# Kernel tuning notes

Measured on AMD Instinct MI355X. Metric: run time of the kernel, lower is better.

## Reference

```python
import jax, jax.numpy as jnp
import numpy as np

TEMPERATURE = 0.1  # init arg `temperature`


def _l2_normalize(x):
    return x / jnp.sqrt(jnp.sum(x * x, axis=1, keepdims=True))


def setup_inputs() -> dict:
    key = jax.random.key(0)
    k1, k2, k3 = jax.random.split(key, 3)
    B, D, Q = 2048, 128, 65536
    projections_1 = jax.random.normal(k1, (B, D), dtype=jnp.float32)
    projections_2 = jax.random.normal(k2, (B, D), dtype=jnp.float32)
    # queue is initialized row-l2-normalized in the original module
    feature_queue = _l2_normalize(jax.random.normal(k3, (Q, D), dtype=jnp.float32))
    return {"projections_1": projections_1, "projections_2": projections_2,
            "feature_queue": feature_queue}


def reference(projections_1, projections_2, feature_queue):
    # NNCLR.contrastive_loss (per-sample losses), including nearest_neighbour.
    p1 = _l2_normalize(projections_1)  # [B, D]
    p2 = _l2_normalize(projections_2)  # [B, D]

    def nearest_neighbour(p):
        # [B, Q] similarity -> top-1 index -> gather from queue
        sims = jnp.einsum('bd,qd->bq', p, feature_queue)
        idx = jnp.argmax(sims, axis=1)  # [B]
        nn = feature_queue[idx]         # [B, D]
        # straight-through: value = nn, gradient flows to p
        return p + jax.lax.stop_gradient(nn - p)

    nn1 = nearest_neighbour(p1)
    nn2 = nearest_neighbour(p2)

    s_1_2_1 = jnp.einsum('id,jd->ij', nn1, p2) / TEMPERATURE
    s_1_2_2 = jnp.einsum('id,jd->ij', p2, nn1) / TEMPERATURE
    s_2_1_1 = jnp.einsum('id,jd->ij', nn2, p1) / TEMPERATURE
    s_2_1_2 = jnp.einsum('id,jd->ij', p1, nn2) / TEMPERATURE

    logits = jnp.concatenate([s_1_2_1, s_1_2_2, s_2_1_1, s_2_1_2], axis=0)  # [4B, B]
    B = p1.shape[0]
    labels = jnp.tile(jnp.arange(B), 4)  # [4B]
    logp = jax.nn.log_softmax(logits, axis=1)
    loss = -jnp.take_along_axis(logp, labels[:, None], axis=1)[:, 0]  # [4B]
    return loss
```

## Files before the change

kernel.cpp:

```cpp
#include <hip/hip_runtime.h>

#define S 132
#define SCALE 10.0f
#define EPS_MARGIN 0.008f
#define SROWS_CAP 480
#define ROWCHUNK 48
#define RC_MAX 10
#define STRIP_CAND 256

typedef __attribute__((ext_vector_type(8))) short short8;
typedef __attribute__((ext_vector_type(4))) float floatx4;

#define MFMA16(a, b, c) __builtin_amdgcn_mfma_f32_16x16x32_bf16((a), (b), (c), 0, 0, 0)

__device__ __forceinline__ unsigned int ordered_bits(float f) {
    unsigned int b = __float_as_uint(f);
    return (b & 0x80000000u) ? ~b : (b | 0x80000000u);
}
__device__ __forceinline__ float from_ordered(unsigned int u) {
    return __uint_as_float((u & 0x80000000u) ? (u ^ 0x80000000u) : ~u);
}
__device__ __forceinline__ short bf_rne(float x) {
    unsigned int u = __float_as_uint(x);
    return (short)((u + 0x7FFFu + ((u >> 16) & 1u)) >> 16);
}
__device__ __forceinline__ float bf2f(short s) {
    return __uint_as_float(((unsigned int)(unsigned short)s) << 16);
}

__global__ void k_prep(const float* __restrict__ p1, const float* __restrict__ p2,
                       float* __restrict__ pn, short* __restrict__ pnb,
                       unsigned int* __restrict__ mbest,
                       unsigned long long* __restrict__ best,
                       unsigned int* __restrict__ scnt,
                       float* __restrict__ sums) {
    int row = blockIdx.x;
    int t = threadIdx.x;
    const float* src = (row < 2048) ? (p1 + (size_t)row * 128)
                                    : (p2 + (size_t)(row - 2048) * 128);
    float2 v = ((const float2*)src)[t];
    float ss = v.x * v.x + v.y * v.y;
    #pragma unroll
    for (int o = 32; o; o >>= 1) ss += __shfl_xor(ss, o);
    float inv = 1.0f / sqrtf(ss);
    float2 o2; o2.x = v.x * inv; o2.y = v.y * inv;
    ((float2*)(pn + (size_t)row * 128))[t] = o2;
    unsigned int pk = (unsigned int)(unsigned short)bf_rne(o2.x)
                    | ((unsigned int)(unsigned short)bf_rne(o2.y) << 16);
    ((unsigned int*)(pnb + (size_t)row * 128))[t] = pk;
    if (t == 0) { mbest[row] = 0u; best[row] = 0ULL; if (row < 1024) scnt[row] = 0u; }
    if (row < 128) sums[row * 64 + t] = 0.0f;
}

__global__ void k_qcvt(const float* __restrict__ queue, short* __restrict__ qb) {
    size_t i = ((size_t)blockIdx.x * 256 + threadIdx.x) * 8;
    float4 f0 = *(const float4*)(queue + i);
    float4 f1 = *(const float4*)(queue + i + 4);
    short8 o;
    o[0] = bf_rne(f0.x); o[1] = bf_rne(f0.y); o[2] = bf_rne(f0.z); o[3] = bf_rne(f0.w);
    o[4] = bf_rne(f1.x); o[5] = bf_rne(f1.y); o[6] = bf_rne(f1.z); o[7] = bf_rne(f1.w);
    *(short8*)(qb + i) = o;
}

__device__ __forceinline__ void screen_tile(const short8 A[8][4],
                                            short8 b0, short8 b1, short8 b2, short8 b3,
                                            float rmax[8][4]) {
    floatx4 acc[8];
    floatx4 zero = {0.0f, 0.0f, 0.0f, 0.0f};
    #pragma unroll
    for (int rf = 0; rf < 8; ++rf) acc[rf] = MFMA16(A[rf][0], b0, zero);
    #pragma unroll
    for (int rf = 0; rf < 8; ++rf) acc[rf] = MFMA16(A[rf][1], b1, acc[rf]);
    #pragma unroll
    for (int rf = 0; rf < 8; ++rf) acc[rf] = MFMA16(A[rf][2], b2, acc[rf]);
    #pragma unroll
    for (int rf = 0; rf < 8; ++rf) acc[rf] = MFMA16(A[rf][3], b3, acc[rf]);
    #pragma unroll
    for (int rf = 0; rf < 8; ++rf)
        #pragma unroll
        for (int r = 0; r < 4; ++r) rmax[rf][r] = fmaxf(rmax[rf][r], acc[rf][r]);
}

__global__ __launch_bounds__(256, 2) void k_screen(const short* __restrict__ pnb,
                                                   const short* __restrict__ qb,
                                                   unsigned int* __restrict__ mbest,
                                                   float* __restrict__ smax) {
    int tid = threadIdx.x;
    int lane = tid & 63, wv = tid >> 6;
    int n16 = lane & 15, quad = lane >> 4;

    int id = blockIdx.x;
    int xcd = id & 7;
    int g = id >> 3;
    int rowblk = g & 7;
    int qsub = g >> 3;
    int qsplit = xcd * 8 + qsub;
    int rowbase = rowblk * 512 + wv * 128;
    int qstart = qsplit * 1024;

    short8 A[8][4];
    #pragma unroll
    for (int rf = 0; rf < 8; ++rf) {
        const short* ap = pnb + (size_t)(rowbase + rf * 16 + n16) * 128 + quad * 8;
        #pragma unroll
        for (int kk = 0; kk < 4; ++kk)
            A[rf][kk] = *(const short8*)(ap + kk * 32);
    }

    float rmax[8][4];
    #pragma unroll
    for (int rf = 0; rf < 8; ++rf)
        #pragma unroll
        for (int r = 0; r < 4; ++r) rmax[rf][r] = -1e30f;

    const short* lp = qb + (size_t)(qstart + n16) * 128 + quad * 8;
    short8 a0 = *(const short8*)(lp), a1 = *(const short8*)(lp + 32),
           a2 = *(const short8*)(lp + 64), a3 = *(const short8*)(lp + 96);

    for (int t = 0; t < 64; t += 2) {
        if ((t & 15) == 0) __syncthreads();
        const short* p1p = lp + 2048;
        short8 b0 = *(const short8*)(p1p), b1 = *(const short8*)(p1p + 32),
               b2 = *(const short8*)(p1p + 64), b3 = *(const short8*)(p1p + 96);
        screen_tile(A, a0, a1, a2, a3, rmax);
        const short* p2p = lp + 4096;
        a0 = *(const short8*)(p2p); a1 = *(const short8*)(p2p + 32);
        a2 = *(const short8*)(p2p + 64); a3 = *(const short8*)(p2p + 96);
        screen_tile(A, b0, b1, b2, b3, rmax);
        lp += 4096;
    }

    #pragma unroll
    for (int rf = 0; rf < 8; ++rf)
        #pragma unroll
        for (int r = 0; r < 4; ++r) {
            float v = rmax[rf][r];
            v = fmaxf(v, __shfl_xor(v, 1));
            v = fmaxf(v, __shfl_xor(v, 2));
            v = fmaxf(v, __shfl_xor(v, 4));
            v = fmaxf(v, __shfl_xor(v, 8));
            if (n16 == 0) {
                int row = rowbase + rf * 16 + quad * 4 + r;
                atomicMax(&mbest[row], ordered_bits(v));
                smax[(size_t)qsplit * 4096 + row] = v;
            }
        }
}

__global__ __launch_bounds__(256) void k_rows(const unsigned int* __restrict__ mbest,
                                              const float* __restrict__ smax,
                                              int* __restrict__ rcnt,
                                              unsigned short* __restrict__ rlist) {
    __shared__ unsigned short rows[SROWS_CAP];
    __shared__ int nsh;
    int tid = threadIdx.x;
    int s = blockIdx.x;
    if (tid == 0) nsh = 0;
    __syncthreads();
    const float* sm = smax + (size_t)s * 4096;
    #pragma unroll
    for (int j = 0; j < 16; ++j) {
        int row = tid + 256 * j;
        float thr = from_ordered(mbest[row]) - EPS_MARGIN;
        if (sm[row] > thr) {
            int pos = atomicAdd(&nsh, 1);
            if (pos < SROWS_CAP) rows[pos] = (unsigned short)row;
        }
    }
    __syncthreads();
    int n = nsh; if (n > SROWS_CAP) n = SROWS_CAP;
    if (tid == 0) rcnt[s] = n;
    for (int i = tid; i < n; i += 256) rlist[s * SROWS_CAP + i] = rows[i];
}

__global__ __launch_bounds__(256, 4) void k_rescreen(const short* __restrict__ pnb,
                                                     const short* __restrict__ qb,
                                                     const unsigned int* __restrict__ mbest,
                                                     const int* __restrict__ rcnt,
                                                     const unsigned short* __restrict__ rlist,
                                                     unsigned int* __restrict__ scnt,
                                                     unsigned int* __restrict__ cand) {
    int b = blockIdx.x;
    int s = b & 63;
    int qp = (b >> 6) & 15;
    int rc = b >> 10;
    int n = rcnt[s];
    int base = rc * ROWCHUNK;
    if (base >= n) return;

    int tid = threadIdx.x;
    int lane = tid & 63, wv = tid >> 6;
    int n16 = lane & 15, quad = lane >> 4;
    int qt = qp * 4 + wv;
    int qrow = s * 1024 + qt * 16 + n16;

    const short* bp = qb + (size_t)qrow * 128 + quad * 8;
    short8 b0 = *(const short8*)(bp);
    short8 b1 = *(const short8*)(bp + 32);
    short8 b2 = *(const short8*)(bp + 64);
    short8 b3 = *(const short8*)(bp + 96);

    const unsigned short* rl = rlist + s * SROWS_CAP;
    short8 Af[3][4]; float th[3][4]; int rowC[3][4];
    #pragma unroll
    for (int rt = 0; rt < 3; ++rt) {
        int ia = base + rt * 16 + n16;
        int rA = rl[ia < n ? ia : base];
        const short* ap = pnb + (size_t)rA * 128 + quad * 8;
        #pragma unroll
        for (int kk = 0; kk < 4; ++kk) Af[rt][kk] = *(const short8*)(ap + kk * 32);
        #pragma unroll
        for (int r = 0; r < 4; ++r) {
            int ic = base + rt * 16 + quad * 4 + r;
            if (ic < n) {
                int rr = rl[ic];
                rowC[rt][r] = rr;
                th[rt][r] = from_ordered(mbest[rr]) - EPS_MARGIN;
            } else { rowC[rt][r] = 0; th[rt][r] = 3.0e38f; }
        }
    }
    #pragma unroll
    for (int rt = 0; rt < 3; ++rt) {
        floatx4 zero = {0.0f, 0.0f, 0.0f, 0.0f};
        floatx4 acc = MFMA16(Af[rt][0], b0, zero);
        acc = MFMA16(Af[rt][1], b1, acc);
        acc = MFMA16(Af[rt][2], b2, acc);
        acc = MFMA16(Af[rt][3], b3, acc);
        #pragma unroll
        for (int r = 0; r < 4; ++r) {
            if (acc[r] > th[rt][r]) {
                unsigned int pos = atomicAdd(&scnt[s * 16], 1u);
                if (pos < STRIP_CAND)
                    cand[s * STRIP_CAND + pos] =
                        ((unsigned int)rowC[rt][r] << 16) | (unsigned int)(qrow & 0xFFFF);
            }
        }
    }
}

__global__ void k_rerank(const float* __restrict__ pn, const float* __restrict__ queue,
                         const unsigned int* __restrict__ scnt,
                         const unsigned int* __restrict__ cand,
                         unsigned long long* __restrict__ best) {
    int widx = (blockIdx.x * 256 + threadIdx.x) >> 6;
    int lane = threadIdx.x & 63;
    int s = widx >> 8, slot = widx & 255;
    unsigned int c = scnt[s * 16]; if (c > STRIP_CAND) c = STRIP_CAND;
    if ((unsigned int)slot >= c) return;
    unsigned int v = cand[s * STRIP_CAND + slot];
    unsigned int row = v >> 16;
    unsigned int q = (unsigned int)(s * 1024) + (v & 0x3FFu);
    q = (unsigned int)(s * 1024) + ((v & 0xFFFFu) - (unsigned int)(s * 1024 & 0xFFFF));
    q = v & 0xFFFFu;
    float2 a = ((const float2*)(pn + (size_t)row * 128))[lane];
    float2 b = ((const float2*)(queue + (size_t)q * 128))[lane];
    float d = a.x * b.x + a.y * b.y;
    #pragma unroll
    for (int o = 32; o; o >>= 1) d += __shfl_xor(d, o);
    if (lane == 0) {
        unsigned long long pk = ((unsigned long long)ordered_bits(d) << 32)
                              | (unsigned long long)(unsigned int)(~q);
        atomicMax(&best[row], pk);
    }
}

__global__ void k_gather(const float* __restrict__ queue,
                         const unsigned long long* __restrict__ best,
                         short* __restrict__ nnb) {
    int row = blockIdx.x;
    int t = threadIdx.x;
    unsigned int idx = ~(unsigned int)(best[row] & 0xFFFFFFFFull);
    idx &= 0xFFFFu;
    float2 v = ((const float2*)(queue + (size_t)idx * 128))[t];
    unsigned int pk = (unsigned int)(unsigned short)bf_rne(v.x)
                    | ((unsigned int)(unsigned short)bf_rne(v.y) << 16);
    ((unsigned int*)(nnb + (size_t)row * 128))[t] = pk;
}

__global__ __launch_bounds__(256) void k_gemm_lse(const short* __restrict__ Ab,
                                                  const float* __restrict__ B,
                                                  float* __restrict__ rowsum,
                                                  float* __restrict__ colsum,
                                                  float* __restrict__ diag) {
    __shared__ __align__(16) float al[64 * S];
    __shared__ __align__(16) float bl[64 * S];
    __shared__ float red[64][17];
    int tid = threadIdx.x;
    const short8* asrc = (const short8*)(Ab + (size_t)blockIdx.x * 64 * 128);
    #pragma unroll
    for (int i = tid; i < 1024; i += 256) {
        short8 v = asrc[i];
        int r = i >> 4, c = (i & 15) * 8;
        float* dst = &al[r * S + c];
        #pragma unroll
        for (int j = 0; j < 8; ++j) dst[j] = bf2f(v[j]);
    }
    const float4* bsrc = (const float4*)(B + (size_t)blockIdx.y * 64 * 128);
    #pragma unroll
    for (int i = tid; i < 2048; i += 256) {
        int r = i >> 5, c = i & 31;
        *(float4*)&bl[r * S + c * 4] = bsrc[i];
    }
    __syncthreads();
    int ty = tid >> 4, tx = tid & 15;
    float acc[4][4] = {};
    #pragma unroll 2
    for (int k = 0; k < 128; k += 4) {
        float4 a[4], b[4];
        #pragma unroll
        for (int i = 0; i < 4; ++i) a[i] = *(const float4*)&al[(ty + 16 * i) * S + k];
        #pragma unroll
        for (int j = 0; j < 4; ++j) b[j] = *(const float4*)&bl[(tx + 16 * j) * S + k];
        #pragma unroll
        for (int i = 0; i < 4; ++i)
            #pragma unroll
            for (int j = 0; j < 4; ++j)
                acc[i][j] += a[i].x * b[j].x + a[i].y * b[j].y +
                             a[i].z * b[j].z + a[i].w * b[j].w;
    }
    int rowbase = blockIdx.x * 64, colbase = blockIdx.y * 64;

    float e[4][4], rs[4], cs[4];
    #pragma unroll
    for (int i = 0; i < 4; ++i) { rs[i] = 0.0f; cs[i] = 0.0f; }
    #pragma unroll
    for (int i = 0; i < 4; ++i)
        #pragma unroll
        for (int j = 0; j < 4; ++j) {
            e[i][j] = __expf(acc[i][j] * SCALE - 10.0f);
            rs[i] += e[i][j];
        }
    #pragma unroll
    for (int j = 0; j < 4; ++j)
        #pragma unroll
        for (int i = 0; i < 4; ++i) cs[j] += e[i][j];

    if (rowbase == colbase && ty == tx) {
        #pragma unroll
        for (int i = 0; i < 4; ++i) diag[rowbase + ty + 16 * i] = acc[i][i];
    }

    #pragma unroll
    for (int i = 0; i < 4; ++i) red[ty + 16 * i][tx] = rs[i];
    __syncthreads();
    if (tid < 64) {
        float s = 0.0f;
        #pragma unroll
        for (int x = 0; x < 16; ++x) s += red[tid][x];
        atomicAdd(&rowsum[rowbase + tid], s);
    }
    __syncthreads();
    #pragma unroll
    for (int j = 0; j < 4; ++j) red[tx + 16 * j][ty] = cs[j];
    __syncthreads();
    if (tid < 64) {
        float s = 0.0f;
        #pragma unroll
        for (int x = 0; x < 16; ++x) s += red[tid][x];
        atomicAdd(&colsum[colbase + tid], s);
    }
}

__global__ void k_final(const float* __restrict__ sums,
                        const float* __restrict__ dg1, const float* __restrict__ dg2,
                        float* __restrict__ out) {
    int idx = blockIdx.x * 256 + threadIdx.x;
    int seg = idx >> 11, r = idx & 2047;
    float s = sums[seg * 2048 + r];
    float d = (seg < 2) ? dg1[r] : dg2[r];
    out[idx] = 10.0f + logf(s) - d * SCALE;
}

extern "C" void kernel_launch(void* const* d_in, const int* in_sizes, int n_in,
                              void* d_out, int out_size, void* d_ws, size_t ws_size,
                              hipStream_t stream) {
    const float* p1    = (const float*)d_in[0];
    const float* p2    = (const float*)d_in[1];
    const float* queue = (const float*)d_in[2];
    float* out = (float*)d_out;

    char* w = (char*)d_ws;
    float* pn  = (float*)w;
    short* nnb = (short*)(w + (2u << 20));
    short* qb  = (short*)(w + (3u << 20));
    short* pnb = (short*)(w + (19u << 20));
    char* b2 = w + (20u << 20);
    unsigned int* mbest = (unsigned int*)b2;
    unsigned long long* best = (unsigned long long*)(b2 + (16u << 10));
    unsigned int* scnt = (unsigned int*)(b2 + (48u << 10));
    int* rcnt = (int*)(b2 + (52u << 10));
    unsigned short* rlist = (unsigned short*)(b2 + (56u << 10));
    unsigned int* cand = (unsigned int*)(b2 + (116u << 10));
    float* sums = (float*)(b2 + (180u << 10));
    float* dg1  = sums + 8192;
    float* dg2  = dg1 + 2048;
    float* smax = (float*)nnb;

    k_prep<<<4096, 64, 0, stream>>>(p1, p2, pn, pnb, mbest, best, scnt, sums);
    k_qcvt<<<4096, 256, 0, stream>>>(queue, qb);
    k_screen<<<512, 256, 0, stream>>>(pnb, qb, mbest, smax);
    k_rows<<<64, 256, 0, stream>>>(mbest, smax, rcnt, rlist);
    k_rescreen<<<64 * 16 * RC_MAX, 256, 0, stream>>>(pnb, qb, mbest, rcnt, rlist, scnt, cand);
    k_rerank<<<4096, 256, 0, stream>>>(pn, queue, scnt, cand, best);
    k_gather<<<4096, 64, 0, stream>>>(queue, best, nnb);

    k_gemm_lse<<<dim3(32, 32), 256, 0, stream>>>(nnb, pn + 2048 * 128,
                                                 sums, sums + 2048, dg1);
    k_gemm_lse<<<dim3(32, 32), 256, 0, stream>>>(nnb + 2048 * 128, pn,
                                                 sums + 4096, sums + 6144, dg2);
    k_final<<<32, 256, 0, stream>>>(sums, dg1, dg2, out);
}
```

Baseline: 247.2 us.

## Rebalance screen, rescreen and rerank grids for occupancy and fewer empty blocks

Result: slower. 302.8 us (+22.5%).

```diff
diff --git a/kernel.cpp b/kernel.cpp
--- a/kernel.cpp
+++ b/kernel.cpp
@@ -5,7 +5,6 @@
 #define EPS_MARGIN 0.008f
 #define SROWS_CAP 480
 #define ROWCHUNK 48
-#define RC_MAX 10
 #define STRIP_CAND 256
 
 typedef __attribute__((ext_vector_type(8))) short short8;
@@ -62,26 +61,7 @@
     *(short8*)(qb + i) = o;
 }
 
-__device__ __forceinline__ void screen_tile(const short8 A[8][4],
-                                            short8 b0, short8 b1, short8 b2, short8 b3,
-                                            float rmax[8][4]) {
-    floatx4 acc[8];
-    floatx4 zero = {0.0f, 0.0f, 0.0f, 0.0f};
-    #pragma unroll
-    for (int rf = 0; rf < 8; ++rf) acc[rf] = MFMA16(A[rf][0], b0, zero);
-    #pragma unroll
-    for (int rf = 0; rf < 8; ++rf) acc[rf] = MFMA16(A[rf][1], b1, acc[rf]);
-    #pragma unroll
-    for (int rf = 0; rf < 8; ++rf) acc[rf] = MFMA16(A[rf][2], b2, acc[rf]);
-    #pragma unroll
-    for (int rf = 0; rf < 8; ++rf) acc[rf] = MFMA16(A[rf][3], b3, acc[rf]);
-    #pragma unroll
-    for (int rf = 0; rf < 8; ++rf)
-        #pragma unroll
-        for (int r = 0; r < 4; ++r) rmax[rf][r] = fmaxf(rmax[rf][r], acc[rf][r]);
-}
-
-__global__ __launch_bounds__(256, 2) void k_screen(const short* __restrict__ pnb,
+__global__ __launch_bounds__(256, 4) void k_screen(const short* __restrict__ pnb,
                                                    const short* __restrict__ qb,
                                                    unsigned int* __restrict__ mbest,
                                                    float* __restrict__ smax) {
@@ -92,46 +72,57 @@
     int id = blockIdx.x;
     int xcd = id & 7;
     int g = id >> 3;
-    int rowblk = g & 7;
-    int qsub = g >> 3;
+    int qsub = g & 7;
+    int rowblk = g >> 3;
     int qsplit = xcd * 8 + qsub;
-    int rowbase = rowblk * 512 + wv * 128;
+    int rowbase = rowblk * 256 + wv * 64;
     int qstart = qsplit * 1024;
 
-    short8 A[8][4];
-    #pragma unroll
-    for (int rf = 0; rf < 8; ++rf) {
+    short8 A[4][4];
+    #pragma unroll
+    for (int rf = 0; rf < 4; ++rf) {
         const short* ap = pnb + (size_t)(rowbase + rf * 16 + n16) * 128 + quad * 8;
         #pragma unroll
         for (int kk = 0; kk < 4; ++kk)
             A[rf][kk] = *(const short8*)(ap + kk * 32);
     }
 
-    float rmax[8][4];
-    #pragma unroll
-    for (int rf = 0; rf < 8; ++rf)
+    float rmax[4][4];
+    #pragma unroll
+    for (int rf = 0; rf < 4; ++rf)
         #pragma unroll
         for (int r = 0; r < 4; ++r) rmax[rf][r] = -1e30f;
 
     const short* lp = qb + (size_t)(qstart + n16) * 128 + quad * 8;
-    short8 a0 = *(const short8*)(lp), a1 = *(const short8*)(lp + 32),
-           a2 = *(const short8*)(lp + 64), a3 = *(const short8*)(lp + 96);
-
-    for (int t = 0; t < 64; t += 2) {
-        if ((t & 15) == 0) __syncthreads();
-        const short* p1p = lp + 2048;
-        short8 b0 = *(const short8*)(p1p), b1 = *(const short8*)(p1p + 32),
-               b2 = *(const short8*)(p1p + 64), b3 = *(const short8*)(p1p + 96);
-        screen_tile(A, a0, a1, a2, a3, rmax);
-        const short* p2p = lp + 4096;
-        a0 = *(const short8*)(p2p); a1 = *(const short8*)(p2p + 32);
-        a2 = *(const short8*)(p2p + 64); a3 = *(const short8*)(p2p + 96);
-        screen_tile(A, b0, b1, b2, b3, rmax);
-        lp += 4096;
-    }
-
-    #pragma unroll
-    for (int rf = 0; rf < 8; ++rf)
+    for (int tb = 0; tb < 4; ++tb) {
+        __syncthreads();
+        #pragma unroll 1
+        for (int ti = 0; ti < 16; ++ti) {
+            short8 b0 = *(const short8*)(lp);
+            short8 b1 = *(const short8*)(lp + 32);
+            short8 b2 = *(const short8*)(lp + 64);
+            short8 b3 = *(const short8*)(lp + 96);
+            floatx4 acc[4];
+            floatx4 zero = {0.0f, 0.0f, 0.0f, 0.0f};
+            #pragma unroll
+            for (int rf = 0; rf < 4; ++rf) acc[rf] = MFMA16(A[rf][0], b0, zero);
+            #pragma unroll
+            for (int rf = 0; rf < 4; ++rf) acc[rf] = MFMA16(A[rf][1], b1, acc[rf]);
+            #pragma unroll
+            for (int rf = 0; rf < 4; ++rf) acc[rf] = MFMA16(A[rf][2], b2, acc[rf]);
+            #pragma unroll
+            for (int rf = 0; rf < 4; ++rf) acc[rf] = MFMA16(A[rf][3], b3, acc[rf]);
+            #pragma unroll
+            for (int rf = 0; rf < 4; ++rf)
+                #pragma unroll
+                for (int r = 0; r < 4; ++r)
+                    rmax[rf][r] = fmaxf(rmax[rf][r], acc[rf][r]);
+            lp += 2048;
+        }
+    }
+
+    #pragma unroll
+    for (int rf = 0; rf < 4; ++rf)
         #pragma unroll
         for (int r = 0; r < 4; ++r) {
             float v = rmax[rf][r];
@@ -182,11 +173,9 @@
                                                      unsigned int* __restrict__ cand) {
     int b = blockIdx.x;
     int s = b & 63;
-    int qp = (b >> 6) & 15;
-    int rc = b >> 10;
+    int qp = b >> 6;
     int n = rcnt[s];
-    int base = rc * ROWCHUNK;
-    if (base >= n) return;
+    if (n == 0) return;
 
     int tid = threadIdx.x;
     int lane = tid & 63, wv = tid >> 6;
@@ -201,38 +190,40 @@
     short8 b3 = *(const short8*)(bp + 96);
 
     const unsigned short* rl = rlist + s * SROWS_CAP;
-    short8 Af[3][4]; float th[3][4]; int rowC[3][4];
-    #pragma unroll
-    for (int rt = 0; rt < 3; ++rt) {
-        int ia = base + rt * 16 + n16;
-        int rA = rl[ia < n ? ia : base];
-        const short* ap = pnb + (size_t)rA * 128 + quad * 8;
-        #pragma unroll
-        for (int kk = 0; kk < 4; ++kk) Af[rt][kk] = *(const short8*)(ap + kk * 32);
-        #pragma unroll
-        for (int r = 0; r < 4; ++r) {
-            int ic = base + rt * 16 + quad * 4 + r;
-            if (ic < n) {
-                int rr = rl[ic];
-                rowC[rt][r] = rr;
-                th[rt][r] = from_ordered(mbest[rr]) - EPS_MARGIN;
-            } else { rowC[rt][r] = 0; th[rt][r] = 3.0e38f; }
-        }
-    }
-    #pragma unroll
-    for (int rt = 0; rt < 3; ++rt) {
-        floatx4 zero = {0.0f, 0.0f, 0.0f, 0.0f};
-        floatx4 acc = MFMA16(Af[rt][0], b0, zero);
-        acc = MFMA16(Af[rt][1], b1, acc);
-        acc = MFMA16(Af[rt][2], b2, acc);
-        acc = MFMA16(Af[rt][3], b3, acc);
-        #pragma unroll
-        for (int r = 0; r < 4; ++r) {
-            if (acc[r] > th[rt][r]) {
-                unsigned int pos = atomicAdd(&scnt[s * 16], 1u);
-                if (pos < STRIP_CAND)
-                    cand[s * STRIP_CAND + pos] =
-                        ((unsigned int)rowC[rt][r] << 16) | (unsigned int)(qrow & 0xFFFF);
+    for (int base = 0; base < n; base += ROWCHUNK) {
+        short8 Af[3][4]; float th[3][4]; int rowC[3][4];
+        #pragma unroll
+        for (int rt = 0; rt < 3; ++rt) {
+            int ia = base + rt * 16 + n16;
+            int rA = rl[ia < n ? ia : base];
+            const short* ap = pnb + (size_t)rA * 128 + quad * 8;
+            #pragma unroll
+            for (int kk = 0; kk < 4; ++kk) Af[rt][kk] = *(const short8*)(ap + kk * 32);
+            #pragma unroll
+            for (int r = 0; r < 4; ++r) {
+                int ic = base + rt * 16 + quad * 4 + r;
+                if (ic < n) {
+                    int rr = rl[ic];
+                    rowC[rt][r] = rr;
+                    th[rt][r] = from_ordered(mbest[rr]) - EPS_MARGIN;
+                } else { rowC[rt][r] = 0; th[rt][r] = 3.0e38f; }
+            }
+        }
+        #pragma unroll
+        for (int rt = 0; rt < 3; ++rt) {
+            floatx4 zero = {0.0f, 0.0f, 0.0f, 0.0f};
+            floatx4 acc = MFMA16(Af[rt][0], b0, zero);
+            acc = MFMA16(Af[rt][1], b1, acc);
+            acc = MFMA16(Af[rt][2], b2, acc);
+            acc = MFMA16(Af[rt][3], b3, acc);
+            #pragma unroll
+            for (int r = 0; r < 4; ++r) {
+                if (acc[r] > th[rt][r]) {
+                    unsigned int pos = atomicAdd(&scnt[s * 16], 1u);
+                    if (pos < STRIP_CAND)
+                        cand[s * STRIP_CAND + pos] =
+                            ((unsigned int)rowC[rt][r] << 16) | (unsigned int)(qrow & 0xFFFF);
+                }
             }
         }
     }
@@ -242,25 +233,24 @@
                          const unsigned int* __restrict__ scnt,
                          const unsigned int* __restrict__ cand,
                          unsigned long long* __restrict__ best) {
-    int widx = (blockIdx.x * 256 + threadIdx.x) >> 6;
-    int lane = threadIdx.x & 63;
-    int s = widx >> 8, slot = widx & 255;
+    int lane = threadIdx.x & 63, wv = threadIdx.x >> 6;
+    int s = blockIdx.x >> 2;
+    int wq = ((blockIdx.x & 3) << 2) | wv;
     unsigned int c = scnt[s * 16]; if (c > STRIP_CAND) c = STRIP_CAND;
-    if ((unsigned int)slot >= c) return;
-    unsigned int v = cand[s * STRIP_CAND + slot];
-    unsigned int row = v >> 16;
-    unsigned int q = (unsigned int)(s * 1024) + (v & 0x3FFu);
-    q = (unsigned int)(s * 1024) + ((v & 0xFFFFu) - (unsigned int)(s * 1024 & 0xFFFF));
-    q = v & 0xFFFFu;
-    float2 a = ((const float2*)(pn + (size_t)row * 128))[lane];
-    float2 b = ((const float2*)(queue + (size_t)q * 128))[lane];
-    float d = a.x * b.x + a.y * b.y;
-    #pragma unroll
-    for (int o = 32; o; o >>= 1) d += __shfl_xor(d, o);
-    if (lane == 0) {
-        unsigned long long pk = ((unsigned long long)ordered_bits(d) << 32)
-                              | (unsigned long long)(unsigned int)(~q);
-        atomicMax(&best[row], pk);
+    for (unsigned int slot = wq; slot < c; slot += 16) {
+        unsigned int v = cand[s * STRIP_CAND + slot];
+        unsigned int row = v >> 16;
+        unsigned int q = v & 0xFFFFu;
+        float2 a = ((const float2*)(pn + (size_t)row * 128))[lane];
+        float2 b = ((const float2*)(queue + (size_t)q * 128))[lane];
+        float d = a.x * b.x + a.y * b.y;
+        #pragma unroll
+        for (int o = 32; o; o >>= 1) d += __shfl_xor(d, o);
+        if (lane == 0) {
+            unsigned long long pk = ((unsigned long long)ordered_bits(d) << 32)
+                                  | (unsigned long long)(unsigned int)(~q);
+            atomicMax(&best[row], pk);
+        }
     }
 }
 
@@ -398,10 +388,10 @@
 
     k_prep<<<4096, 64, 0, stream>>>(p1, p2, pn, pnb, mbest, best, scnt, sums);
     k_qcvt<<<4096, 256, 0, stream>>>(queue, qb);
-    k_screen<<<512, 256, 0, stream>>>(pnb, qb, mbest, smax);
+    k_screen<<<1024, 256, 0, stream>>>(pnb, qb, mbest, smax);
     k_rows<<<64, 256, 0, stream>>>(mbest, smax, rcnt, rlist);
-    k_rescreen<<<64 * 16 * RC_MAX, 256, 0, stream>>>(pnb, qb, mbest, rcnt, rlist, scnt, cand);
-    k_rerank<<<4096, 256, 0, stream>>>(pn, queue, scnt, cand, best);
+    k_rescreen<<<64 * 16, 256, 0, stream>>>(pnb, qb, mbest, rcnt, rlist, scnt, cand);
+    k_rerank<<<256, 256, 0, stream>>>(pn, queue, scnt, cand, best);
     k_gather<<<4096, 64, 0, stream>>>(queue, best, nnb);
 
     k_gemm_lse<<<dim3(32, 32), 256, 0, stream>>>(nnb, pn + 2048 * 128,
```
